# Kernel optimization log

Hardware: AMD Instinct MI355X
Metric: run time of the kernel (lower is better)

## Reference

```python
import jax, jax.numpy as jnp
import numpy as np

N = 4096        # nodes (atoms)
E = 65536       # edges (avg degree 16)
H = 128         # hidden_channels
R = 32          # num_rbf
MAX_Z = 128
CUTOFF_UPPER = 4.5
LN_EPS = 1e-5


def _linear_params(key, out_f, in_f, bias=True, scale=None):
    kw, kb = jax.random.split(key)
    s = scale if scale is not None else (1.0 / np.sqrt(in_f))
    W = jax.random.uniform(kw, (out_f, in_f), jnp.float32, -s, s)
    if bias:
        b = jax.random.uniform(kb, (out_f,), jnp.float32, -s, s)
        return W, b
    return W


def setup_inputs() -> dict:
    key = jax.random.key(0)
    ks = jax.random.split(key, 24)
    z = jax.random.randint(ks[0], (N,), 0, MAX_Z)
    edge_index = jax.random.randint(ks[1], (2, E), 0, N)
    edge_weight = jax.random.uniform(ks[2], (E,), jnp.float32) * CUTOFF_UPPER
    ev = jax.random.normal(ks[3], (E, 3), jnp.float32)
    edge_vec_norm = ev / jnp.linalg.norm(ev, axis=-1, keepdims=True)
    edge_attr = jax.random.uniform(ks[4], (E, R), jnp.float32)
    labels = jax.random.normal(ks[5], (N,), jnp.float32)
    labels_mask = jax.random.randint(ks[6], (N,), 0, 2).astype(bool)

    emb_w = jax.random.normal(ks[7], (MAX_Z, H), jnp.float32)  # nn.Embedding default N(0,1)
    emb2_w, emb2_b = _linear_params(ks[8], H, 2 * H)
    label_emb_w, label_emb_b = _linear_params(ks[9], H, 1)
    label_emb2_w, label_emb2_b = _linear_params(ks[10], H, 2 * H)
    mask_token = jax.random.normal(ks[11], (H,), jnp.float32)
    dp1_w, dp1_b = _linear_params(ks[12], H, R)
    dp2_w, dp2_b = _linear_params(ks[13], H, R)
    dp3_w, dp3_b = _linear_params(ks[14], H, R)
    lt0_w = _linear_params(ks[15], H, H, bias=False)
    lt1_w = _linear_params(ks[16], H, H, bias=False)
    lt2_w = _linear_params(ks[17], H, H, bias=False)
    ls1_w, ls1_b = _linear_params(ks[18], 2 * H, H)
    ls2_w, ls2_b = _linear_params(ks[19], 3 * H, 2 * H)
    ln_g = jnp.ones((H,), jnp.float32)
    ln_b = jnp.zeros((H,), jnp.float32)

    return dict(z=z, edge_index=edge_index, edge_weight=edge_weight,
                edge_vec_norm=edge_vec_norm, edge_attr=edge_attr,
                labels=labels, labels_mask=labels_mask,
                emb_w=emb_w, emb2_w=emb2_w, emb2_b=emb2_b,
                label_emb_w=label_emb_w, label_emb_b=label_emb_b,
                mask_token=mask_token,
                label_emb2_w=label_emb2_w, label_emb2_b=label_emb2_b,
                dp1_w=dp1_w, dp1_b=dp1_b, dp2_w=dp2_w, dp2_b=dp2_b,
                dp3_w=dp3_w, dp3_b=dp3_b,
                lt0_w=lt0_w, lt1_w=lt1_w, lt2_w=lt2_w,
                ls1_w=ls1_w, ls1_b=ls1_b, ls2_w=ls2_w, ls2_b=ls2_b,
                ln_g=ln_g, ln_b=ln_b)


def _cosine_cutoff(d):
    # cutoff_lower == 0 branch of CosineCutoff
    c = 0.5 * (jnp.cos(d * (np.pi / CUTOFF_UPPER)) + 1.0)
    return c * (d < CUTOFF_UPPER).astype(d.dtype)


def _skewtensor(v):
    zero = jnp.zeros_like(v[:, 0])
    t = jnp.stack([zero, -v[:, 2], v[:, 1],
                   v[:, 2], zero, -v[:, 0],
                   -v[:, 1], v[:, 0], zero], axis=1)
    return t.reshape(-1, 3, 3)


def _symtensor(v):
    vv = v[:, :, None] * v[:, None, :]               # [E,3,3], symmetric
    tr = jnp.trace(vv, axis1=-2, axis2=-1) / 3.0     # mean of diagonal
    eye = jnp.eye(3, dtype=v.dtype)
    return vv - tr[:, None, None] * eye              # traceless symmetric part


def _layernorm(x, g, b):
    mu = jnp.mean(x, axis=-1, keepdims=True)
    var = jnp.mean(jnp.square(x - mu), axis=-1, keepdims=True)
    return (x - mu) * jax.lax.rsqrt(var + LN_EPS) * g + b


def reference(z, edge_index, edge_weight, edge_vec_norm, edge_attr, labels,
              labels_mask, emb_w, emb2_w, emb2_b, label_emb_w, label_emb_b,
              mask_token, label_emb2_w, label_emb2_b, dp1_w, dp1_b, dp2_w,
              dp2_b, dp3_w, dp3_b, lt0_w, lt1_w, lt2_w, ls1_w, ls1_b, ls2_w,
              ls2_b, ln_g, ln_b):
    src, dst = edge_index[0], edge_index[1]
    n = z.shape[0]

    # --- atomic-number message: Zij = emb2(concat(Z[src], Z[dst])) ---
    Z = emb_w[z]                                                   # [N,H]
    Zij = jnp.concatenate([Z[src], Z[dst]], -1) @ emb2_w.T + emb2_b  # [E,H]

    # --- label message with mask-token substitution ---
    L = labels[:, None] @ label_emb_w.T + label_emb_b              # [N,H]
    L = jnp.where(labels_mask[:, None], mask_token, L)
    Lij = jnp.concatenate([L[src], L[dst]], -1) @ label_emb2_w.T + label_emb2_b

    # --- tensor messages ---
    CZ = _cosine_cutoff(edge_weight)[:, None] * (Zij + Lij)        # [E,H]
    eye = jnp.eye(3, dtype=edge_vec_norm.dtype)
    f1 = edge_attr @ dp1_w.T + dp1_b                               # [E,H]
    f2 = edge_attr @ dp2_w.T + dp2_b
    f3 = edge_attr @ dp3_w.T + dp3_b
    skew = _skewtensor(edge_vec_norm)                              # [E,3,3]
    sym = _symtensor(edge_vec_norm)                                # [E,3,3]
    Iij = (f1 * CZ)[:, :, None, None] * eye                        # [E,H,3,3]
    Aij = (f2 * CZ)[:, :, None, None] * skew[:, None]
    Sij = (f3 * CZ)[:, :, None, None] * sym[:, None]

    # --- scatter-add into node tensors ---
    I = jax.ops.segment_sum(Iij, src, num_segments=n)              # [N,H,3,3]
    A = jax.ops.segment_sum(Aij, src, num_segments=n)
    S = jax.ops.segment_sum(Sij, src, num_segments=n)

    # --- norm + scalar MLP gating ---
    X3 = I + A + S
    norm = jnp.sum(jnp.square(X3), axis=(-2, -1))                  # tensor_norm -> [N,H]
    norm = _layernorm(norm, ln_g, ln_b)
    norm = jax.nn.silu(norm @ ls1_w.T + ls1_b)                     # [N,2H]
    norm = jax.nn.silu(norm @ ls2_w.T + ls2_b)                     # [N,3H]
    norm = norm.reshape(n, -1, 3)                                  # [N,H,3]

    # --- channel-mixing linears over hidden dim, gated per component ---
    I = jnp.einsum('nhij,gh->ngij', I, lt0_w) * norm[:, :, 0, None, None]
    A = jnp.einsum('nhij,gh->ngij', A, lt1_w) * norm[:, :, 1, None, None]
    S = jnp.einsum('nhij,gh->ngij', S, lt2_w) * norm[:, :, 2, None, None]
    return I + A + S                                               # [N,H,3,3]
```

## Files before the change

### kernel.cpp

```cpp
#include <hip/hip_runtime.h>
#include <hip/hip_bf16.h>
#include <math.h>

#define NN 4096
#define EE 65536
#define HH 128
#define RR 32
#define MAXZ 128
#define CUT 4.5f
#define PI_OVER_CUT 0.6981317007977318f
#define LN_EPS 1e-5f

typedef unsigned short u16;
typedef unsigned int u32;
typedef unsigned char u8;
typedef _Float16 h2 __attribute__((ext_vector_type(2)));
typedef _Float16 hf8 __attribute__((ext_vector_type(8)));
typedef float f32x4 __attribute__((ext_vector_type(4)));

__device__ __forceinline__ float dot4(float4 a, float4 b){
    return a.x*b.x + a.y*b.y + a.z*b.z + a.w*b.w;
}
__device__ __forceinline__ float silu(float x){ return x / (1.f + __expf(-x)); }
__device__ __forceinline__ u32 packh2(float a, float b){
    union{u32 u; h2 h;} v; v.h = (h2){(_Float16)a, (_Float16)b}; return v.u;
}
__device__ __forceinline__ float fdot2u(u32 a, u32 b, float c){
    union{u32 u; h2 h;} x, y; x.u = a; y.u = b;
    return __builtin_amdgcn_fdot2(x.h, y.h, c, false);
}
__device__ __forceinline__ u16 f2h(float f){
    union{u16 u; _Float16 h;} v; v.h = (_Float16)f; return v.u;
}
__device__ __forceinline__ float h2f(u16 u){
    union{u16 u_; _Float16 h;} v; v.u_ = u; return (float)v.h;
}

__global__ void k_sig(float* __restrict__ out, float val, int n){
    int i = blockIdx.x*256 + threadIdx.x;
    if (i < n) out[i] = val;
}

__global__ void k_zero(int* __restrict__ deg){
    deg[blockIdx.x*256 + threadIdx.x] = 0;
}

__global__ __launch_bounds__(256) void k_cvt(const u8* __restrict__ zr,
                                             const u8* __restrict__ eir,
                                             const u8* __restrict__ mr,
                                             int* __restrict__ z32,
                                             int* __restrict__ ei32,
                                             int* __restrict__ m32,
                                             int* __restrict__ deg,
                                             const float* __restrict__ emb_w,
                                             const float* __restrict__ emb2_w,
                                             const float* __restrict__ label_emb_w,
                                             const float* __restrict__ label_emb_b,
                                             const float* __restrict__ mask_token,
                                             const float* __restrict__ label_emb2_w,
                                             const float* __restrict__ label_emb2_b,
                                             const float* __restrict__ emb2_b,
                                             float* __restrict__ PzA,
                                             float* __restrict__ PzB,
                                             float* __restrict__ vecs){
    int b = blockIdx.x, t = threadIdx.x;
    if (b < 512){
        __shared__ int sF1, sF3, sOdd, sZ64, sE64;
        if (t == 0){ sF1=0; sF3=0; sOdd=0; sZ64=1; sE64=1; }
        __syncthreads();
        for (int i = t; i < 4096; i += 256){
            u8 bb = mr[i];
            if ((i & 3) == 1 && bb == 0x3F) sF1 = 1;
            if ((i & 3) == 3 && bb == 0x3F) sF3 = 1;
            if ((i & 3) != 0 && bb != 0)    sOdd = 1;
        }
        const u32* zw = (const u32*)zr;
        const u32* ew = (const u32*)eir;
        for (int i = t; i < 128; i += 256) if (zw[2*i + 1]) sZ64 = 0;
        for (int i = t; i < 512; i += 256) if (ew[2*i + 1]) sE64 = 0;
        __syncthreads();
        int mf = sF1 ? 2 : (sF3 ? 0 : (sOdd ? 1 : 0));
        int z64 = sZ64, e64 = sE64;

        int i = b*256 + t;
        if (i < NN){
            z32[i] = z64 ? ((const int*)zr)[2*i] : ((const int*)zr)[i];
            int mm;
            if (mf == 1)      mm = (mr[i] != 0);
            else if (mf == 2) mm = (((const u16*)mr)[i] != 0);
            else              mm = (((const u32*)mr)[i] != 0u);
            m32[i] = mm;
        }
        if (i < 2*EE){
            int v = e64 ? ((const int*)eir)[2*i] : ((const int*)eir)[i];
            ei32[i] = v;
            if (i < EE) atomicAdd(&deg[v], 1);
        }
        return;
    }
    if (b < 576){
        int zi = (b - 512)*2 + (t >> 7), h = t & 127;
        __shared__ float Zs[2][HH];
        Zs[t >> 7][h] = emb_w[zi*HH + h];
        __syncthreads();
        const float4* wa = (const float4*)(emb2_w + h*2*HH);
        const float4* wb = (const float4*)(emb2_w + h*2*HH + HH);
        float pa = 0.f, pbv = 0.f;
        const float* Z = Zs[t >> 7];
        #pragma unroll 8
        for (int j = 0; j < HH/4; ++j){
            float4 zp = *(const float4*)&Z[4*j];
            pa  += dot4(wa[j], zp);
            pbv += dot4(wb[j], zp);
        }
        PzA[zi*HH + h] = pa;
        PzB[zi*HH + h] = pbv;
        return;
    }
    if (t < 128){
        int h = t;
        const float* wa = label_emb2_w + h*2*HH;
        const float* wb = wa + HH;
        float uA=0.f,vA=0.f,wA=0.f,uB=0.f,vB=0.f,wB=0.f;
        for (int j = 0; j < HH; ++j){
            float a = wa[j], bb = wb[j];
            float u = label_emb_w[j], v = label_emb_b[j], m = mask_token[j];
            uA += a*u; vA += a*v; wA += a*m;
            uB += bb*u; vB += bb*v; wB += bb*m;
        }
        float bias = emb2_b[h] + label_emb2_b[h];
        vecs[0*HH + h] = uA;
        vecs[1*HH + h] = vA + bias;
        vecs[2*HH + h] = wA + bias;
        vecs[3*HH + h] = uB;
        vecs[4*HH + h] = vB;
        vecs[5*HH + h] = wB;
    }
}

__global__ __launch_bounds__(256) void k_scan(const int* __restrict__ deg,
                                              int* __restrict__ offsets,
                                              int* __restrict__ cursor){
    int t = threadIdx.x;
    int lane = t & 63, wid = t >> 6;
    int4 d[4];
    #pragma unroll
    for (int q = 0; q < 4; ++q) d[q] = ((const int4*)deg)[t*4 + q];
    int vals[16];
    #pragma unroll
    for (int q = 0; q < 4; ++q){
        vals[4*q+0]=d[q].x; vals[4*q+1]=d[q].y; vals[4*q+2]=d[q].z; vals[4*q+3]=d[q].w;
    }
    int sum = 0;
    #pragma unroll
    for (int q = 0; q < 16; ++q) sum += vals[q];
    int incl = sum;
    #pragma unroll
    for (int dd = 1; dd < 64; dd <<= 1){ int s = __shfl_up(incl, dd); if (lane >= dd) incl += s; }
    __shared__ int wsum[4];
    if (lane == 63) wsum[wid] = incl;
    __syncthreads();
    int base = 0;
    for (int w = 0; w < wid; ++w) base += wsum[w];
    int run = base + incl - sum;
    #pragma unroll
    for (int q = 0; q < 16; ++q){
        offsets[t*16 + q] = run;
        cursor [t*16 + q] = run;
        run += vals[q];
    }
    if (t == 255) offsets[NN] = run;
}

__global__ __launch_bounds__(256) void k_sp(
    const int* __restrict__ ei, int* __restrict__ cursor,
    const float* __restrict__ ew, const float* __restrict__ ev,
    const float* __restrict__ ea,
    u32* __restrict__ attrSh, int* __restrict__ dstA, float4* __restrict__ metaA,
    const float* __restrict__ ls1_w, const float* __restrict__ ls2_w,
    const float* __restrict__ lt0_w, const float* __restrict__ lt1_w,
    const float* __restrict__ lt2_w,
    const float* __restrict__ dp1_w, const float* __restrict__ dp2_w,
    const float* __restrict__ dp3_w,
    u16* __restrict__ ls1H, u16* __restrict__ ls2H, u16* __restrict__ ltH,
    u32* __restrict__ dpTh,
    const int* __restrict__ z32, const int* __restrict__ m32,
    const float* __restrict__ labels,
    const float* __restrict__ PzA, const float* __restrict__ PzB,
    const float* __restrict__ vecs,
    float* __restrict__ Pa, u16* __restrict__ Pbh)
{
    int b = blockIdx.x, t = threadIdx.x;
    if (b < 256){
        int e = b*256 + t;
        int s = ei[e];
        int p = atomicAdd(&cursor[s], 1);
        float d = ew[e];
        float cutv = (d < CUT) ? 0.5f*(__cosf(d*PI_OVER_CUT) + 1.f) : 0.f;
        dstA[p] = ei[EE + e];
        metaA[p] = make_float4(cutv, ev[3*e], ev[3*e+1], ev[3*e+2]);
        const float* a = ea + (size_t)e*RR;
        u32* o = attrSh + (size_t)p*16;
        #pragma unroll
        for (int q = 0; q < 16; ++q)
            o[q] = packh2(cutv*a[2*q], cutv*a[2*q+1]);
        return;
    }
    int pb = b - 256;
    if (pb < 728){
        int i = pb*256 + t;
        if (i < 32768){ ls1H[i] = f2h(ls1_w[i]); return; }
        i -= 32768;
        if (i < 98304){ ls2H[i] = f2h(ls2_w[i]); return; }
        i -= 98304;
        if (i < 16384){ ltH[0*16384 + i] = f2h(lt0_w[i]); return; }
        i -= 16384;
        if (i < 16384){ ltH[1*16384 + i] = f2h(lt1_w[i]); return; }
        i -= 16384;
        if (i < 16384){ ltH[2*16384 + i] = f2h(lt2_w[i]); return; }
        i -= 16384;
        if (i < 6144){
            int j = i >> 11, rem = i & 2047, q = rem >> 7, h = rem & 127;
            const float* src = (j == 0) ? dp1_w : ((j == 1) ? dp2_w : dp3_w);
            dpTh[(j*16 + q)*HH + h] = packh2(src[h*RR + 2*q], src[h*RR + 2*q + 1]);
            return;
        }
        return;
    }
    int i = (b - 984)*256 + t;
    int n = i >> 7, h = i & 127;
    int zi = z32[n];
    int mk = m32[n];
    float lab = labels[n];
    float la = mk ? vecs[2*HH + h] : lab*vecs[0*HH + h] + vecs[1*HH + h];
    float lb = mk ? vecs[5*HH + h] : lab*vecs[3*HH + h] + vecs[4*HH + h];
    Pa[i]  = PzA[zi*HH + h] + la;
    Pbh[i] = f2h(PzB[zi*HH + h] + lb);
}

__global__ __launch_bounds__(128) void k_gather(
    const u32* __restrict__ attrSh, const int* __restrict__ dstA,
    const float4* __restrict__ metaA,
    const u32* __restrict__ dpTh,
    const float* __restrict__ dp1_b, const float* __restrict__ dp2_b,
    const float* __restrict__ dp3_b,
    const float* __restrict__ Pa, const u16* __restrict__ Pbh,
    const int* __restrict__ offsets,
    u16* __restrict__ X0, u16* __restrict__ X1, u16* __restrict__ X2,
    float* __restrict__ norm2)
{
    int n = blockIdx.x, t = threadIdx.x;
    u32 w1[16], w2[16], w3[16];
    #pragma unroll
    for (int q = 0; q < 16; ++q){
        w1[q] = dpTh[(0*16 + q)*HH + t];
        w2[q] = dpTh[(1*16 + q)*HH + t];
        w3[q] = dpTh[(2*16 + q)*HH + t];
    }
    float fb1 = dp1_b[t], fb2 = dp2_b[t], fb3 = dp3_b[t];
    float pa = Pa[n*HH + t];
    float ai = 0.f, aw0 = 0.f, aw1 = 0.f, aw2 = 0.f;
    float m00 = 0.f, m01 = 0.f, m02 = 0.f, m11 = 0.f, m12 = 0.f, m22 = 0.f;

    int e0 = offsets[n], e1 = offsets[n+1];
    int j = e0;
    for (; j + 1 < e1; j += 2){
        int dsta = dstA[j], dstb = dstA[j+1];
        float4 ma = metaA[j], mb = metaA[j+1];
        float sa = pa + h2f(Pbh[(size_t)dsta*HH + t]);
        float sb = pa + h2f(Pbh[(size_t)dstb*HH + t]);
        const u32* Aa = attrSh + (size_t)j*16;
        const u32* Ab = Aa + 16;
        float f1a = ma.x*fb1, f2a = ma.x*fb2, f3a = ma.x*fb3;
        float f1b = mb.x*fb1, f2b = mb.x*fb2, f3b = mb.x*fb3;
        #pragma unroll
        for (int q = 0; q < 16; ++q){
            u32 a = Aa[q], bq = Ab[q];
            f1a = fdot2u(a, w1[q], f1a);
            f2a = fdot2u(a, w2[q], f2a);
            f3a = fdot2u(a, w3[q], f3a);
            f1b = fdot2u(bq, w1[q], f1b);
            f2b = fdot2u(bq, w2[q], f2b);
            f3b = fdot2u(bq, w3[q], f3b);
        }
        float aa = f1a*sa, ba = f2a*sa, ca = f3a*sa;
        float ab = f1b*sb, bb = f2b*sb, cb = f3b*sb;
        ai  += aa;            ai  += ab;
        aw0 += ba*ma.y;       aw0 += bb*mb.y;
        aw1 += ba*ma.z;       aw1 += bb*mb.z;
        aw2 += ba*ma.w;       aw2 += bb*mb.w;
        float cva0 = ca*ma.y, cva1 = ca*ma.z;
        float cvb0 = cb*mb.y, cvb1 = cb*mb.z;
        m00 += cva0*ma.y;     m00 += cvb0*mb.y;
        m01 += cva0*ma.z;     m01 += cvb0*mb.z;
        m02 += cva0*ma.w;     m02 += cvb0*mb.w;
        m11 += cva1*ma.z;     m11 += cvb1*mb.z;
        m12 += cva1*ma.w;     m12 += cvb1*mb.w;
        m22 += ca*ma.w*ma.w;  m22 += cb*mb.w*mb.w;
    }
    if (j < e1){
        int dst = dstA[j];
        float4 m4 = metaA[j];
        float s = pa + h2f(Pbh[(size_t)dst*HH + t]);
        const u32* Aa = attrSh + (size_t)j*16;
        float f1 = m4.x*fb1, f2 = m4.x*fb2, f3 = m4.x*fb3;
        #pragma unroll
        for (int q = 0; q < 16; ++q){
            u32 a = Aa[q];
            f1 = fdot2u(a, w1[q], f1);
            f2 = fdot2u(a, w2[q], f2);
            f3 = fdot2u(a, w3[q], f3);
        }
        float a = f1*s, b = f2*s, c = f3*s;
        ai  += a;
        aw0 += b*m4.y; aw1 += b*m4.z; aw2 += b*m4.w;
        float cv0 = c*m4.y, cv1 = c*m4.z;
        m00 += cv0*m4.y; m01 += cv0*m4.z; m02 += cv0*m4.w;
        m11 += cv1*m4.z; m12 += cv1*m4.w; m22 += c*m4.w*m4.w;
    }

    X0[(size_t)n*HH + t] = f2h(ai);
    u16* x1p = X1 + (size_t)3*n*HH + t;
    x1p[0*HH] = f2h(aw0); x1p[1*HH] = f2h(aw1); x1p[2*HH] = f2h(aw2);
    u16* x2p = X2 + (size_t)6*n*HH + t;
    x2p[0*HH] = f2h(m00); x2p[1*HH] = f2h(m01); x2p[2*HH] = f2h(m02);
    x2p[3*HH] = f2h(m11); x2p[4*HH] = f2h(m12); x2p[5*HH] = f2h(m22);

    float tr3 = (m00 + m11 + m22) * (1.f/3.f);
    float x00 = ai + m00 - tr3, x11 = ai + m11 - tr3, x22 = ai + m22 - tr3;
    float nn = x00*x00 + x11*x11 + x22*x22
             + 2.f*(m01*m01 + aw2*aw2 + m02*m02 + aw1*aw1 + m12*m12 + aw0*aw0);
    norm2[n*HH + t] = nn;
}

__global__ __launch_bounds__(512) void k_tail(
    const float* __restrict__ norm2, const float* __restrict__ ln_g,
    const float* __restrict__ ln_b,
    const u16* __restrict__ ls1H, const float* __restrict__ ls1_b,
    const u16* __restrict__ ls2H, const float* __restrict__ ls2_b,
    float* __restrict__ gates,
    const u16* __restrict__ X0, const u16* __restrict__ X1,
    const u16* __restrict__ X2, const u16* __restrict__ ltH,
    float* __restrict__ out)
{
    int n0 = blockIdx.x * 16;
    int t = threadIdx.x;
    int wave = t >> 6, lane = t & 63;
    int rlo = lane & 15, kb = lane >> 4;
    __shared__ u16 ysH[16][136];
    __shared__ u16 usH[16][264];
    __shared__ u16 Yl[160*136];

    hf8 a0[4], a1[4];
    {
        int tile = wave;
        const u16* X; int rbase;
        if (tile == 0)     { X = X0; rbase = n0; }
        else if (tile < 4) { X = X1; rbase = 3*n0 + (tile-1)*16; }
        else               { X = X2; rbase = 6*n0 + (tile-4)*16; }
        const hf8* xr = (const hf8*)(X + (size_t)(rbase + rlo)*HH + kb*8);
        #pragma unroll
        for (int ks = 0; ks < 4; ++ks) a0[ks] = xr[ks*4];
    }
    if (wave < 2){
        int tile = wave + 8;
        int rbase = 6*n0 + (tile-4)*16;
        const hf8* xr = (const hf8*)(X2 + (size_t)(rbase + rlo)*HH + kb*8);
        #pragma unroll
        for (int ks = 0; ks < 4; ++ks) a1[ks] = xr[ks*4];
    }

    if (wave < 4){
        int ni = wave*4 + kb;
        int n = n0 + ni;
        float x[8]; float s = 0.f;
        #pragma unroll
        for (int k = 0; k < 8; ++k){ x[k] = norm2[(size_t)n*HH + rlo + 16*k]; s += x[k]; }
        #pragma unroll
        for (int d = 1; d < 16; d <<= 1) s += __shfl_xor(s, d);
        float mu = s * (1.f/HH);
        float q = 0.f;
        #pragma unroll
        for (int k = 0; k < 8; ++k){ float dx = x[k]-mu; q += dx*dx; }
        #pragma unroll
        for (int d = 1; d < 16; d <<= 1) q += __shfl_xor(q, d);
        float rs = rsqrtf(q*(1.f/HH) + LN_EPS);
        #pragma unroll
        for (int k = 0; k < 8; ++k){
            int h = rlo + 16*k;
            ysH[ni][h] = f2h((x[k]-mu)*rs*ln_g[h] + ln_b[h]);
        }
    }
    __syncthreads();

    {
        hf8 a[4];
        #pragma unroll
        for (int ks = 0; ks < 4; ++ks)
            a[ks] = *(const hf8*)&ysH[rlo][kb*8 + ks*32];
        for (int ct = wave; ct < 16; ct += 8){
            f32x4 acc = (f32x4){0.f,0.f,0.f,0.f};
            const u16* wr0 = ls1H + (size_t)(ct*16 + rlo)*HH;
            #pragma unroll
            for (int ks = 0; ks < 4; ++ks){
                hf8 bf = *(const hf8*)(wr0 + kb*8 + ks*32);
                acc = __builtin_amdgcn_mfma_f32_16x16x32_f16(a[ks], bf, acc, 0, 0, 0);
            }
            float bias = ls1_b[ct*16 + rlo];
            #pragma unroll
            for (int j = 0; j < 4; ++j)
                usH[kb*4 + j][ct*16 + rlo] = f2h(silu(acc[j] + bias));
        }
    }
    __syncthreads();

    {
        hf8 a[8];
        #pragma unroll
        for (int ks = 0; ks < 8; ++ks)
            a[ks] = *(const hf8*)&usH[rlo][kb*8 + ks*32];
        for (int ct = wave; ct < 24; ct += 8){
            f32x4 acc = (f32x4){0.f,0.f,0.f,0.f};
            const u16* wr0 = ls2H + (size_t)(ct*16 + rlo)*256;
            #pragma unroll
            for (int ks = 0; ks < 8; ++ks){
                hf8 bf = *(const hf8*)(wr0 + kb*8 + ks*32);
                acc = __builtin_amdgcn_mfma_f32_16x16x32_f16(a[ks], bf, acc, 0, 0, 0);
            }
            float bias = ls2_b[ct*16 + rlo];
            #pragma unroll
            for (int j = 0; j < 4; ++j){
                int n = n0 + kb*4 + j;
                gates[(size_t)n*384 + ct*16 + rlo] = silu(acc[j] + bias);
            }
        }
    }

    {
        int tile = wave;
        const u16* W = (tile == 0) ? ltH : ((tile < 4) ? ltH + 16384 : ltH + 32768);
        #pragma unroll
        for (int ct = 0; ct < 8; ++ct){
            f32x4 acc = (f32x4){0.f,0.f,0.f,0.f};
            const hf8* wr = (const hf8*)(W + (size_t)(ct*16 + rlo)*HH + kb*8);
            #pragma unroll
            for (int ks = 0; ks < 4; ++ks)
                acc = __builtin_amdgcn_mfma_f32_16x16x32_f16(a0[ks], wr[ks*4], acc, 0, 0, 0);
            #pragma unroll
            for (int j = 0; j < 4; ++j)
                Yl[(tile*16 + kb*4 + j)*136 + ct*16 + rlo] = f2h(acc[j]);
        }
    }
    if (wave < 2){
        int tile = wave + 8;
        const u16* W = ltH + 32768;
        #pragma unroll
        for (int ct = 0; ct < 8; ++ct){
            f32x4 acc = (f32x4){0.f,0.f,0.f,0.f};
            const hf8* wr = (const hf8*)(W + (size_t)(ct*16 + rlo)*HH + kb*8);
            #pragma unroll
            for (int ks = 0; ks < 4; ++ks)
                acc = __builtin_amdgcn_mfma_f32_16x16x32_f16(a1[ks], wr[ks*4], acc, 0, 0, 0);
            #pragma unroll
            for (int j = 0; j < 4; ++j)
                Yl[(tile*16 + kb*4 + j)*136 + ct*16 + rlo] = f2h(acc[j]);
        }
    }
    __syncthreads();

    #pragma unroll
    for (int q = 0; q < 4; ++q){
        int id = q*512 + t;
        int ni = id >> 7, g = id & 127;
        int n = n0 + ni;
        float mi  = h2f(Yl[ni*136 + g]);
        float mw0 = h2f(Yl[(16 + 3*ni + 0)*136 + g]);
        float mw1 = h2f(Yl[(16 + 3*ni + 1)*136 + g]);
        float mw2 = h2f(Yl[(16 + 3*ni + 2)*136 + g]);
        float mm0 = h2f(Yl[(64 + 6*ni + 0)*136 + g]);
        float mm1 = h2f(Yl[(64 + 6*ni + 1)*136 + g]);
        float mm2 = h2f(Yl[(64 + 6*ni + 2)*136 + g]);
        float mm3 = h2f(Yl[(64 + 6*ni + 3)*136 + g]);
        float mm4 = h2f(Yl[(64 + 6*ni + 4)*136 + g]);
        float mm5 = h2f(Yl[(64 + 6*ni + 5)*136 + g]);
        float g0 = gates[(size_t)n*384 + 3*g];
        float g1 = gates[(size_t)n*384 + 3*g + 1];
        float g2 = gates[(size_t)n*384 + 3*g + 2];
        float t3 = (mm0 + mm3 + mm5) * (1.f/3.f);
        float* op = out + ((size_t)n*HH + g)*9;
        op[0] =  g0*mi  + g2*(mm0 - t3);
        op[1] = -g1*mw2 + g2*mm1;
        op[2] =  g1*mw1 + g2*mm2;
        op[3] =  g1*mw2 + g2*mm1;
        op[4] =  g0*mi  + g2*(mm3 - t3);
        op[5] = -g1*mw0 + g2*mm4;
        op[6] = -g1*mw1 + g2*mm2;
        op[7] =  g1*mw0 + g2*mm4;
        op[8] =  g0*mi  + g2*(mm5 - t3);
    }
}

extern "C" void kernel_launch(void* const* d_in, const int* in_sizes, int n_in,
                              void* d_out, int out_size, void* d_ws, size_t ws_size,
                              hipStream_t stream)
{
    float* out = (float*)d_out;
    int sig_blocks = (out_size + 255)/256;

    if (out_size != NN*HH*9){
        k_sig<<<sig_blocks, 256, 0, stream>>>(out, 400.f, out_size);
        return;
    }
    if (n_in != 30){
        k_sig<<<sig_blocks, 256, 0, stream>>>(out, 300.f + (float)n_in, out_size);
        return;
    }
    static const int want[30] = {
        4096, 131072, 65536, 196608, 2097152, 4096, 4096,
        16384, 32768, 128, 128, 128, 128, 32768, 128,
        4096, 128, 4096, 128, 4096, 128,
        16384, 16384, 16384, 32768, 256, 98304, 384, 128, 128
    };
    for (int i = 0; i < 30; ++i){
        if (in_sizes[i] != want[i]){
            k_sig<<<sig_blocks, 256, 0, stream>>>(out, 200.f + (float)i, out_size);
            return;
        }
    }

    const u8*    z_raw        = (const u8*)d_in[0];
    const u8*    ei_raw       = (const u8*)d_in[1];
    const float* edge_weight  = (const float*)d_in[2];
    const float* edge_vec     = (const float*)d_in[3];
    const float* edge_attr    = (const float*)d_in[4];
    const float* labels       = (const float*)d_in[5];
    const u8*    mask_raw     = (const u8*)d_in[6];
    const float* emb_w        = (const float*)d_in[7];
    const float* emb2_w       = (const float*)d_in[8];
    const float* emb2_b       = (const float*)d_in[9];
    const float* label_emb_w  = (const float*)d_in[10];
    const float* label_emb_b  = (const float*)d_in[11];
    const float* mask_token   = (const float*)d_in[12];
    const float* label_emb2_w = (const float*)d_in[13];
    const float* label_emb2_b = (const float*)d_in[14];
    const float* dp1_w = (const float*)d_in[15];
    const float* dp1_b = (const float*)d_in[16];
    const float* dp2_w = (const float*)d_in[17];
    const float* dp2_b = (const float*)d_in[18];
    const float* dp3_w = (const float*)d_in[19];
    const float* dp3_b = (const float*)d_in[20];
    const float* lt0_w = (const float*)d_in[21];
    const float* lt1_w = (const float*)d_in[22];
    const float* lt2_w = (const float*)d_in[23];
    const float* ls1_w = (const float*)d_in[24];
    const float* ls1_b = (const float*)d_in[25];
    const float* ls2_w = (const float*)d_in[26];
    const float* ls2_b = (const float*)d_in[27];
    const float* ln_g  = (const float*)d_in[28];
    const float* ln_b  = (const float*)d_in[29];

    char* ws = (char*)d_ws;
    size_t off = 0;
    auto alloc = [&](size_t bytes) -> void* {
        void* p = ws + off;
        off += (bytes + 255) & ~(size_t)255;
        return p;
    };
    float* Pa      = (float*)alloc((size_t)NN*HH*4);
    u16*   Pbh     = (u16*)alloc((size_t)NN*HH*2);
    float* norm2   = (float*)alloc((size_t)NN*HH*4);
    float* gates   = (float*)alloc((size_t)NN*384*4);
    float* PzA     = (float*)alloc((size_t)MAXZ*HH*4);
    float* PzB     = (float*)alloc((size_t)MAXZ*HH*4);
    float* vecs    = (float*)alloc((size_t)6*HH*4);
    u32*   dpTh    = (u32*)alloc((size_t)3*16*HH*4);
    u16*   ls1H    = (u16*)alloc((size_t)32768*2);
    u16*   ls2H    = (u16*)alloc((size_t)98304*2);
    u16*   ltH     = (u16*)alloc((size_t)3*16384*2);
    u16*   X0      = (u16*)alloc((size_t)NN*HH*2);
    u16*   X1      = (u16*)alloc((size_t)3*NN*HH*2);
    u16*   X2      = (u16*)alloc((size_t)6*NN*HH*2);
    u32*   attrSh  = (u32*)alloc((size_t)EE*16*4);
    float* metaA   = (float*)alloc((size_t)EE*16);
    int*   dstA    = (int*)alloc((size_t)EE*4);
    int*   z32     = (int*)alloc((size_t)NN*4);
    int*   ei32    = (int*)alloc((size_t)2*EE*4);
    int*   m32     = (int*)alloc((size_t)NN*4);
    int*   deg     = (int*)alloc((size_t)NN*4);
    int*   offsets = (int*)alloc((size_t)(NN+1)*4);
    int*   cursor  = (int*)alloc((size_t)NN*4);

    if (off > ws_size){
        k_sig<<<sig_blocks, 256, 0, stream>>>(out, 150.f, out_size);
        return;
    }

    k_zero   <<<NN/256, 256, 0, stream>>>(deg);
    k_cvt    <<<577, 256, 0, stream>>>(z_raw, ei_raw, mask_raw,
                                       z32, ei32, m32, deg,
                                       emb_w, emb2_w,
                                       label_emb_w, label_emb_b, mask_token,
                                       label_emb2_w, label_emb2_b, emb2_b,
                                       PzA, PzB, vecs);
    k_scan   <<<1, 256, 0, stream>>>(deg, offsets, cursor);
    k_sp     <<<3032, 256, 0, stream>>>(ei32, cursor, edge_weight, edge_vec,
                                        edge_attr, attrSh, dstA, (float4*)metaA,
                                        ls1_w, ls2_w, lt0_w, lt1_w, lt2_w,
                                        dp1_w, dp2_w, dp3_w,
                                        ls1H, ls2H, ltH, dpTh,
                                        z32, m32, labels, PzA, PzB, vecs,
                                        Pa, Pbh);
    k_gather <<<NN, 128, 0, stream>>>(attrSh, dstA, (const float4*)metaA,
                                      dpTh, dp1_b, dp2_b, dp3_b,
                                      Pa, Pbh, offsets, X0, X1, X2, norm2);
    k_tail   <<<NN/16, 512, 0, stream>>>(norm2, ln_g, ln_b, ls1H, ls1_b,
                                         ls2H, ls2_b, gates,
                                         X0, X1, X2, ltH, out);
}
```

Measured before the change: 88.71 us.

## Fuse edge gather into tail kernel via shared-memory node tensors

Merges the per-node edge gather kernel into the tail kernel. Each 512-thread block first accumulates the 16 nodes it owns into shared memory (Yl and norm2l), then runs the layernorm, MLP and channel-mixing stages from shared memory. This removes the global X0/X1/X2/norm2 round trip and one kernel launch. In exchange the gather phase now runs with only 256 blocks, each thread handles 4 nodes serially, and degree imbalance inside a block can stall the whole block. The 48 weight registers now compete with the tail's register and LDS budget.

Result: slower. 112.3 us (+26.5%).

```diff
diff --git a/kernel.cpp b/kernel.cpp
--- a/kernel.cpp
+++ b/kernel.cpp
@@ -238,7 +238,7 @@
     Pbh[i] = f2h(PzB[zi*HH + h] + lb);
 }
 
-__global__ __launch_bounds__(128) void k_gather(
+__global__ __launch_bounds__(512) void k_gt(
     const u32* __restrict__ attrSh, const int* __restrict__ dstA,
     const float4* __restrict__ metaA,
     const u32* __restrict__ dpTh,
@@ -246,136 +246,135 @@
     const float* __restrict__ dp3_b,
     const float* __restrict__ Pa, const u16* __restrict__ Pbh,
     const int* __restrict__ offsets,
-    u16* __restrict__ X0, u16* __restrict__ X1, u16* __restrict__ X2,
-    float* __restrict__ norm2)
-{
-    int n = blockIdx.x, t = threadIdx.x;
-    u32 w1[16], w2[16], w3[16];
-    #pragma unroll
-    for (int q = 0; q < 16; ++q){
-        w1[q] = dpTh[(0*16 + q)*HH + t];
-        w2[q] = dpTh[(1*16 + q)*HH + t];
-        w3[q] = dpTh[(2*16 + q)*HH + t];
-    }
-    float fb1 = dp1_b[t], fb2 = dp2_b[t], fb3 = dp3_b[t];
-    float pa = Pa[n*HH + t];
-    float ai = 0.f, aw0 = 0.f, aw1 = 0.f, aw2 = 0.f;
-    float m00 = 0.f, m01 = 0.f, m02 = 0.f, m11 = 0.f, m12 = 0.f, m22 = 0.f;
-
-    int e0 = offsets[n], e1 = offsets[n+1];
-    int j = e0;
-    for (; j + 1 < e1; j += 2){
-        int dsta = dstA[j], dstb = dstA[j+1];
-        float4 ma = metaA[j], mb = metaA[j+1];
-        float sa = pa + h2f(Pbh[(size_t)dsta*HH + t]);
-        float sb = pa + h2f(Pbh[(size_t)dstb*HH + t]);
-        const u32* Aa = attrSh + (size_t)j*16;
-        const u32* Ab = Aa + 16;
-        float f1a = ma.x*fb1, f2a = ma.x*fb2, f3a = ma.x*fb3;
-        float f1b = mb.x*fb1, f2b = mb.x*fb2, f3b = mb.x*fb3;
-        #pragma unroll
-        for (int q = 0; q < 16; ++q){
-            u32 a = Aa[q], bq = Ab[q];
-            f1a = fdot2u(a, w1[q], f1a);
-            f2a = fdot2u(a, w2[q], f2a);
-            f3a = fdot2u(a, w3[q], f3a);
-            f1b = fdot2u(bq, w1[q], f1b);
-            f2b = fdot2u(bq, w2[q], f2b);
-            f3b = fdot2u(bq, w3[q], f3b);
-        }
-        float aa = f1a*sa, ba = f2a*sa, ca = f3a*sa;
-        float ab = f1b*sb, bb = f2b*sb, cb = f3b*sb;
-        ai  += aa;            ai  += ab;
-        aw0 += ba*ma.y;       aw0 += bb*mb.y;
-        aw1 += ba*ma.z;       aw1 += bb*mb.z;
-        aw2 += ba*ma.w;       aw2 += bb*mb.w;
-        float cva0 = ca*ma.y, cva1 = ca*ma.z;
-        float cvb0 = cb*mb.y, cvb1 = cb*mb.z;
-        m00 += cva0*ma.y;     m00 += cvb0*mb.y;
-        m01 += cva0*ma.z;     m01 += cvb0*mb.z;
-        m02 += cva0*ma.w;     m02 += cvb0*mb.w;
-        m11 += cva1*ma.z;     m11 += cvb1*mb.z;
-        m12 += cva1*ma.w;     m12 += cvb1*mb.w;
-        m22 += ca*ma.w*ma.w;  m22 += cb*mb.w*mb.w;
-    }
-    if (j < e1){
-        int dst = dstA[j];
-        float4 m4 = metaA[j];
-        float s = pa + h2f(Pbh[(size_t)dst*HH + t]);
-        const u32* Aa = attrSh + (size_t)j*16;
-        float f1 = m4.x*fb1, f2 = m4.x*fb2, f3 = m4.x*fb3;
-        #pragma unroll
-        for (int q = 0; q < 16; ++q){
-            u32 a = Aa[q];
-            f1 = fdot2u(a, w1[q], f1);
-            f2 = fdot2u(a, w2[q], f2);
-            f3 = fdot2u(a, w3[q], f3);
-        }
-        float a = f1*s, b = f2*s, c = f3*s;
-        ai  += a;
-        aw0 += b*m4.y; aw1 += b*m4.z; aw2 += b*m4.w;
-        float cv0 = c*m4.y, cv1 = c*m4.z;
-        m00 += cv0*m4.y; m01 += cv0*m4.z; m02 += cv0*m4.w;
-        m11 += cv1*m4.z; m12 += cv1*m4.w; m22 += c*m4.w*m4.w;
-    }
-
-    X0[(size_t)n*HH + t] = f2h(ai);
-    u16* x1p = X1 + (size_t)3*n*HH + t;
-    x1p[0*HH] = f2h(aw0); x1p[1*HH] = f2h(aw1); x1p[2*HH] = f2h(aw2);
-    u16* x2p = X2 + (size_t)6*n*HH + t;
-    x2p[0*HH] = f2h(m00); x2p[1*HH] = f2h(m01); x2p[2*HH] = f2h(m02);
-    x2p[3*HH] = f2h(m11); x2p[4*HH] = f2h(m12); x2p[5*HH] = f2h(m22);
-
-    float tr3 = (m00 + m11 + m22) * (1.f/3.f);
-    float x00 = ai + m00 - tr3, x11 = ai + m11 - tr3, x22 = ai + m22 - tr3;
-    float nn = x00*x00 + x11*x11 + x22*x22
-             + 2.f*(m01*m01 + aw2*aw2 + m02*m02 + aw1*aw1 + m12*m12 + aw0*aw0);
-    norm2[n*HH + t] = nn;
-}
-
-__global__ __launch_bounds__(512) void k_tail(
-    const float* __restrict__ norm2, const float* __restrict__ ln_g,
-    const float* __restrict__ ln_b,
+    const float* __restrict__ ln_g, const float* __restrict__ ln_b,
     const u16* __restrict__ ls1H, const float* __restrict__ ls1_b,
     const u16* __restrict__ ls2H, const float* __restrict__ ls2_b,
-    float* __restrict__ gates,
-    const u16* __restrict__ X0, const u16* __restrict__ X1,
-    const u16* __restrict__ X2, const u16* __restrict__ ltH,
+    float* __restrict__ gates, const u16* __restrict__ ltH,
     float* __restrict__ out)
 {
     int n0 = blockIdx.x * 16;
     int t = threadIdx.x;
     int wave = t >> 6, lane = t & 63;
     int rlo = lane & 15, kb = lane >> 4;
+    __shared__ u16 Yl[160*136];
     __shared__ u16 ysH[16][136];
     __shared__ u16 usH[16][264];
-    __shared__ u16 Yl[160*136];
+    __shared__ float norm2l[16][128];
+
+    {
+        int h = t & 127;
+        int g = t >> 7;
+        u32 w1[16], w2[16], w3[16];
+        #pragma unroll
+        for (int q = 0; q < 16; ++q){
+            w1[q] = dpTh[(0*16 + q)*HH + h];
+            w2[q] = dpTh[(1*16 + q)*HH + h];
+            w3[q] = dpTh[(2*16 + q)*HH + h];
+        }
+        float fb1 = dp1_b[h], fb2 = dp2_b[h], fb3 = dp3_b[h];
+        for (int it = 0; it < 4; ++it){
+            int ni = g*4 + it;
+            int n = n0 + ni;
+            float pa = Pa[n*HH + h];
+            float ai = 0.f, aw0 = 0.f, aw1 = 0.f, aw2 = 0.f;
+            float m00 = 0.f, m01 = 0.f, m02 = 0.f, m11 = 0.f, m12 = 0.f, m22 = 0.f;
+
+            int e0 = offsets[n], e1 = offsets[n+1];
+            int j = e0;
+            for (; j + 1 < e1; j += 2){
+                int dsta = dstA[j], dstb = dstA[j+1];
+                float4 ma = metaA[j], mb = metaA[j+1];
+                float sa = pa + h2f(Pbh[(size_t)dsta*HH + h]);
+                float sb = pa + h2f(Pbh[(size_t)dstb*HH + h]);
+                const u32* Aa = attrSh + (size_t)j*16;
+                const u32* Ab = Aa + 16;
+                float f1a = ma.x*fb1, f2a = ma.x*fb2, f3a = ma.x*fb3;
+                float f1b = mb.x*fb1, f2b = mb.x*fb2, f3b = mb.x*fb3;
+                #pragma unroll
+                for (int q = 0; q < 16; ++q){
+                    u32 a = Aa[q], bq = Ab[q];
+                    f1a = fdot2u(a, w1[q], f1a);
+                    f2a = fdot2u(a, w2[q], f2a);
+                    f3a = fdot2u(a, w3[q], f3a);
+                    f1b = fdot2u(bq, w1[q], f1b);
+                    f2b = fdot2u(bq, w2[q], f2b);
+                    f3b = fdot2u(bq, w3[q], f3b);
+                }
+                float aa = f1a*sa, ba = f2a*sa, ca = f3a*sa;
+                float ab = f1b*sb, bb = f2b*sb, cb = f3b*sb;
+                ai  += aa;            ai  += ab;
+                aw0 += ba*ma.y;       aw0 += bb*mb.y;
+                aw1 += ba*ma.z;       aw1 += bb*mb.z;
+                aw2 += ba*ma.w;       aw2 += bb*mb.w;
+                float cva0 = ca*ma.y, cva1 = ca*ma.z;
+                float cvb0 = cb*mb.y, cvb1 = cb*mb.z;
+                m00 += cva0*ma.y;     m00 += cvb0*mb.y;
+                m01 += cva0*ma.z;     m01 += cvb0*mb.z;
+                m02 += cva0*ma.w;     m02 += cvb0*mb.w;
+                m11 += cva1*ma.z;     m11 += cvb1*mb.z;
+                m12 += cva1*ma.w;     m12 += cvb1*mb.w;
+                m22 += ca*ma.w*ma.w;  m22 += cb*mb.w*mb.w;
+            }
+            if (j < e1){
+                int dst = dstA[j];
+                float4 m4 = metaA[j];
+                float s = pa + h2f(Pbh[(size_t)dst*HH + h]);
+                const u32* Aa = attrSh + (size_t)j*16;
+                float f1 = m4.x*fb1, f2 = m4.x*fb2, f3 = m4.x*fb3;
+                #pragma unroll
+                for (int q = 0; q < 16; ++q){
+                    u32 a = Aa[q];
+                    f1 = fdot2u(a, w1[q], f1);
+                    f2 = fdot2u(a, w2[q], f2);
+                    f3 = fdot2u(a, w3[q], f3);
+                }
+                float a = f1*s, b = f2*s, c = f3*s;
+                ai  += a;
+                aw0 += b*m4.y; aw1 += b*m4.z; aw2 += b*m4.w;
+                float cv0 = c*m4.y, cv1 = c*m4.z;
+                m00 += cv0*m4.y; m01 += cv0*m4.z; m02 += cv0*m4.w;
+                m11 += cv1*m4.z; m12 += cv1*m4.w; m22 += c*m4.w*m4.w;
+            }
+
+            Yl[(0*16 + ni)*136 + h]     = f2h(ai);
+            Yl[(16 + 3*ni + 0)*136 + h] = f2h(aw0);
+            Yl[(16 + 3*ni + 1)*136 + h] = f2h(aw1);
+            Yl[(16 + 3*ni + 2)*136 + h] = f2h(aw2);
+            Yl[(64 + 6*ni + 0)*136 + h] = f2h(m00);
+            Yl[(64 + 6*ni + 1)*136 + h] = f2h(m01);
+            Yl[(64 + 6*ni + 2)*136 + h] = f2h(m02);
+            Yl[(64 + 6*ni + 3)*136 + h] = f2h(m11);
+            Yl[(64 + 6*ni + 4)*136 + h] = f2h(m12);
+            Yl[(64 + 6*ni + 5)*136 + h] = f2h(m22);
+
+            float tr3 = (m00 + m11 + m22) * (1.f/3.f);
+            float x00 = ai + m00 - tr3, x11 = ai + m11 - tr3, x22 = ai + m22 - tr3;
+            float nn = x00*x00 + x11*x11 + x22*x22
+                     + 2.f*(m01*m01 + aw2*aw2 + m02*m02 + aw1*aw1 + m12*m12 + aw0*aw0);
+            norm2l[ni][h] = nn;
+        }
+    }
+    __syncthreads();
 
     hf8 a0[4], a1[4];
     {
         int tile = wave;
-        const u16* X; int rbase;
-        if (tile == 0)     { X = X0; rbase = n0; }
-        else if (tile < 4) { X = X1; rbase = 3*n0 + (tile-1)*16; }
-        else               { X = X2; rbase = 6*n0 + (tile-4)*16; }
-        const hf8* xr = (const hf8*)(X + (size_t)(rbase + rlo)*HH + kb*8);
-        #pragma unroll
-        for (int ks = 0; ks < 4; ++ks) a0[ks] = xr[ks*4];
+        const u16* xr = &Yl[(tile*16 + rlo)*136 + kb*8];
+        #pragma unroll
+        for (int ks = 0; ks < 4; ++ks) a0[ks] = *(const hf8*)(xr + ks*32);
     }
     if (wave < 2){
         int tile = wave + 8;
-        int rbase = 6*n0 + (tile-4)*16;
-        const hf8* xr = (const hf8*)(X2 + (size_t)(rbase + rlo)*HH + kb*8);
-        #pragma unroll
-        for (int ks = 0; ks < 4; ++ks) a1[ks] = xr[ks*4];
+        const u16* xr = &Yl[(tile*16 + rlo)*136 + kb*8];
+        #pragma unroll
+        for (int ks = 0; ks < 4; ++ks) a1[ks] = *(const hf8*)(xr + ks*32);
     }
 
     if (wave < 4){
         int ni = wave*4 + kb;
-        int n = n0 + ni;
         float x[8]; float s = 0.f;
         #pragma unroll
-        for (int k = 0; k < 8; ++k){ x[k] = norm2[(size_t)n*HH + rlo + 16*k]; s += x[k]; }
+        for (int k = 0; k < 8; ++k){ x[k] = norm2l[ni][rlo + 16*k]; s += x[k]; }
         #pragma unroll
         for (int d = 1; d < 16; d <<= 1) s += __shfl_xor(s, d);
         float mu = s * (1.f/HH);
@@ -568,7 +567,6 @@
     };
     float* Pa      = (float*)alloc((size_t)NN*HH*4);
     u16*   Pbh     = (u16*)alloc((size_t)NN*HH*2);
-    float* norm2   = (float*)alloc((size_t)NN*HH*4);
     float* gates   = (float*)alloc((size_t)NN*384*4);
     float* PzA     = (float*)alloc((size_t)MAXZ*HH*4);
     float* PzB     = (float*)alloc((size_t)MAXZ*HH*4);
@@ -577,9 +575,6 @@
     u16*   ls1H    = (u16*)alloc((size_t)32768*2);
     u16*   ls2H    = (u16*)alloc((size_t)98304*2);
     u16*   ltH     = (u16*)alloc((size_t)3*16384*2);
-    u16*   X0      = (u16*)alloc((size_t)NN*HH*2);
-    u16*   X1      = (u16*)alloc((size_t)3*NN*HH*2);
-    u16*   X2      = (u16*)alloc((size_t)6*NN*HH*2);
     u32*   attrSh  = (u32*)alloc((size_t)EE*16*4);
     float* metaA   = (float*)alloc((size_t)EE*16);
     int*   dstA    = (int*)alloc((size_t)EE*4);
@@ -610,10 +605,9 @@
                                         ls1H, ls2H, ltH, dpTh,
                                         z32, m32, labels, PzA, PzB, vecs,
                                         Pa, Pbh);
-    k_gather <<<NN, 128, 0, stream>>>(attrSh, dstA, (const float4*)metaA,
-                                      dpTh, dp1_b, dp2_b, dp3_b,
-                                      Pa, Pbh, offsets, X0, X1, X2, norm2);
-    k_tail   <<<NN/16, 512, 0, stream>>>(norm2, ln_g, ln_b, ls1H, ls1_b,
-                                         ls2H, ls2_b, gates,
-                                         X0, X1, X2, ltH, out);
-}
+    k_gt     <<<NN/16, 512, 0, stream>>>(attrSh, dstA, (const float4*)metaA,
+                                         dpTh, dp1_b, dp2_b, dp3_b,
+                                         Pa, Pbh, offsets,
+                                         ln_g, ln_b, ls1H, ls1_b,
+                                         ls2H, ls2_b, gates, ltH, out);
+}
```
